# Performance work log

Measured on AMD Instinct MI355X. Metric: run time of the kernel, lower is better.

Reference implementation:

```python
import jax, jax.numpy as jnp
import numpy as np

LOOKUP_WINDOW = 101  # module init arg
EPS = 1e-12  # F.normalize eps


def setup_inputs() -> dict:
    key = jax.random.key(0)
    k1, k2, k3 = jax.random.split(key, 3)
    B, T, F_IN, D = 4, 2048, 2048, 128
    x = jax.random.normal(k1, (B, T, F_IN), dtype=jnp.float32)
    # nn.Linear(in_filters, output_dim); stored here as [in, out] so y = x @ W + b
    W = jax.random.normal(k2, (F_IN, D), dtype=jnp.float32) / np.sqrt(F_IN).astype(np.float32)
    b = jax.random.normal(k3, (D,), dtype=jnp.float32) * 0.01
    return {"x": x, "W": W, "b": b}


def reference(x, W, b):
    hw = LOOKUP_WINDOW // 2
    # projection + L2 normalize over feature dim (F.normalize p=2, dim=-1)
    p = x @ W + b  # [B,T,D]
    p = p / jnp.maximum(jnp.linalg.norm(p, axis=-1, keepdims=True), EPS)
    B, T, D = p.shape
    # zero-pad along time so out-of-range neighbors contribute 0 similarity
    pp = jnp.pad(p, ((0, 0), (hw, hw), (0, 0)))  # [B, T+2*hw, D]
    # window gather: idx[t, w] = t + w indexes padded time axis (neighbor t + w - hw)
    idx = jnp.arange(T)[:, None] + jnp.arange(LOOKUP_WINDOW)[None, :]  # [T, W]
    windows = pp[:, idx, :]  # [B, T, W, D]
    # banded similarity: sim[b,t,w] = <p[b,t], neighbor at offset w-hw>
    sim = jnp.einsum('btd,btwd->btw', p, windows)
    return sim  # [B, T, LOOKUP_WINDOW]
```

## Files before the change

kernel.cpp:

```cpp
#include <hip/hip_runtime.h>
#include <hip/hip_bf16.h>

#define T_LEN 2048
#define D_DIM 128
#define K_DIM 2048
#define M_DIM 8192
#define LOOKUP 101
#define HWIN 50

typedef __attribute__((ext_vector_type(8))) short short8;
typedef __attribute__((ext_vector_type(4))) float f32x4;

static __device__ __forceinline__ unsigned int f2bf(float f) {
  unsigned int u = __float_as_uint(f);
  return (u + 0x7fffu + ((u >> 16) & 1u)) >> 16;
}
static __device__ __forceinline__ float bflo(unsigned int u) { return __uint_as_float(u << 16); }
static __device__ __forceinline__ float bfhi(unsigned int u) { return __uint_as_float(u & 0xffff0000u); }

static __device__ __forceinline__ short8 pack8(float4 lo, float4 hi) {
  uint4 u;
  u.x = f2bf(lo.x) | (f2bf(lo.y) << 16);
  u.y = f2bf(lo.z) | (f2bf(lo.w) << 16);
  u.z = f2bf(hi.x) | (f2bf(hi.y) << 16);
  u.w = f2bf(hi.z) | (f2bf(hi.w) << 16);
  return *(short8*)&u;
}

typedef __attribute__((address_space(3))) unsigned char lds_uchar;
typedef const __attribute__((address_space(1))) unsigned char g_uchar;
static __device__ __forceinline__ void gll16(const void* g, void* l) {
  __builtin_amdgcn_global_load_lds((g_uchar*)g, (lds_uchar*)l, 16, 0, 0);
}

__global__ __launch_bounds__(256) void k_pack(const float* __restrict__ W,
                                              unsigned short* __restrict__ Bp) {
  __shared__ float sw[32][132];
  const int ks = blockIdx.x;
  const int t = threadIdx.x;
  const float* src = W + (size_t)ks * 32 * D_DIM;
#pragma unroll
  for (int j = 0; j < 4; ++j) {
    int idx = t + j * 256;
    int row = idx >> 5, c4 = idx & 31;
    float4 v = *(const float4*)(src + row * D_DIM + c4 * 4);
    *(float4*)&sw[row][c4 * 4] = v;
  }
  __syncthreads();
#pragma unroll
  for (int e = 0; e < 2; ++e) {
    int f = t * 2 + e;
    int ct = f >> 6, l = f & 63;
    int kr = (l >> 4) * 8, col = ct * 16 + (l & 15);
    uint4 o;
    o.x = f2bf(sw[kr + 0][col]) | (f2bf(sw[kr + 1][col]) << 16);
    o.y = f2bf(sw[kr + 2][col]) | (f2bf(sw[kr + 3][col]) << 16);
    o.z = f2bf(sw[kr + 4][col]) | (f2bf(sw[kr + 5][col]) << 16);
    o.w = f2bf(sw[kr + 6][col]) | (f2bf(sw[kr + 7][col]) << 16);
    *(uint4*)(Bp + (((size_t)(ks * 8 + ct) << 6) + l) * 8) = o;
  }
}

__global__ __launch_bounds__(512, 4) void k_gemm(const float* __restrict__ X,
                                                 const unsigned short* __restrict__ Bp,
                                                 const float* __restrict__ bias,
                                                 unsigned short* __restrict__ Pn) {
  __shared__ __align__(16) unsigned char smem[65536];
  const int tid = threadIdx.x;
  const int lane = tid & 63;
  const int wv = tid >> 6;
  const int r0 = blockIdx.x * 16;
  const int l15 = lane & 15;
  const int kg = lane >> 4;

  unsigned char* Ab = smem + wv * 8192;
  const int srow = lane >> 5;
  const int scol = lane & 31;

  f32x4 acc[8];
#pragma unroll
  for (int i = 0; i < 8; ++i) acc[i] = (f32x4){0.f, 0.f, 0.f, 0.f};

  for (int c = 0; c < 2; ++c) {
#pragma unroll
    for (int i = 0; i < 8; ++i) {
      int r = 2 * i + srow;
      int gsrc = scol ^ (r & 7);
      const float* src = X + (size_t)(r0 + r) * K_DIM + wv * 256 + c * 128 + gsrc * 4;
      gll16(src, Ab + i * 1024);
    }
    asm volatile("s_waitcnt vmcnt(0)" ::: "memory");
    __builtin_amdgcn_sched_barrier(0);
#pragma unroll
    for (int s = 0; s < 4; ++s) {
      int g0 = s * 8 + kg * 2;
      float4 alo = *(const float4*)(Ab + l15 * 512 + (((g0 + 0) ^ (l15 & 7)) << 4));
      float4 ahi = *(const float4*)(Ab + l15 * 512 + (((g0 + 1) ^ (l15 & 7)) << 4));
      short8 af = pack8(alo, ahi);
      int ksg = wv * 8 + c * 4 + s;
#pragma unroll
      for (int ct = 0; ct < 8; ++ct) {
        short8 bf = *(const short8*)(Bp + (((size_t)(ksg * 8 + ct) << 6) + lane) * 8);
        acc[ct] = __builtin_amdgcn_mfma_f32_16x16x32_bf16(af, bf, acc[ct], 0, 0, 0);
      }
    }
  }

  float* Pw = (float*)Ab;
#pragma unroll
  for (int ct = 0; ct < 8; ++ct)
#pragma unroll
    for (int j = 0; j < 4; ++j)
      Pw[(kg * 4 + j) * 128 + ct * 16 + l15] = acc[ct][j];
  __syncthreads();

  const int row = tid >> 5;
  const int c4 = tid & 31;
  float4 tot = make_float4(0.f, 0.f, 0.f, 0.f);
#pragma unroll
  for (int q = 0; q < 8; ++q) {
    float4 v = *(const float4*)(smem + q * 8192 + row * 512 + c4 * 16);
    tot.x += v.x; tot.y += v.y; tot.z += v.z; tot.w += v.w;
  }
  float4 bv = *(const float4*)(bias + c4 * 4);
  tot.x += bv.x; tot.y += bv.y; tot.z += bv.z; tot.w += bv.w;
  float ss = tot.x * tot.x + tot.y * tot.y + tot.z * tot.z + tot.w * tot.w;
  ss += __shfl_xor(ss, 1);
  ss += __shfl_xor(ss, 2);
  ss += __shfl_xor(ss, 4);
  ss += __shfl_xor(ss, 8);
  ss += __shfl_xor(ss, 16);
  float sc = 1.0f / fmaxf(sqrtf(ss), 1e-12f);
  unsigned int p0 = f2bf(tot.x * sc) | (f2bf(tot.y * sc) << 16);
  unsigned int p1 = f2bf(tot.z * sc) | (f2bf(tot.w * sc) << 16);
  *(uint2*)(Pn + (size_t)(r0 + row) * D_DIM + c4 * 4) = make_uint2(p0, p1);
}

#define SROWS 144

__global__ __launch_bounds__(256) void k_sim(const unsigned short* __restrict__ Pn,
                                             float* __restrict__ out) {
  __shared__ unsigned short sm[SROWS * D_DIM];
  const int bb = blockIdx.x >> 6;
  const int tb = blockIdx.x & 63;
  const int t0 = tb * 32;
  const int tid = threadIdx.x;

  for (int idx = tid; idx < SROWS * 16; idx += 256) {
    int i = idx >> 4, seg = idx & 15;
    int t = t0 - HWIN + i;
    uint4 val = make_uint4(0u, 0u, 0u, 0u);
    if (t >= 0 && t < T_LEN)
      val = *(const uint4*)(Pn + ((size_t)bb * T_LEN + t) * D_DIM + seg * 8);
    *(uint4*)&sm[i * D_DIM + ((seg ^ (i & 7)) << 3)] = val;
  }
  __syncthreads();

  const int lane = tid & 63;
  const int wv = tid >> 6;
  const int l15 = lane & 15;
  const int kg = lane >> 4;
  const int rt = wv >> 1;
  const int itp = wv & 1;

  short8 af[4];
  const int ia = HWIN + rt * 16 + l15;
#pragma unroll
  for (int ks = 0; ks < 4; ++ks) {
    int g = ks * 4 + kg;
    af[ks] = *(const short8*)&sm[ia * D_DIM + ((g ^ (ia & 7)) << 3)];
  }

  for (int it = itp; it < 9; it += 2) {
    f32x4 acc = (f32x4){0.f, 0.f, 0.f, 0.f};
    const int ib = it * 16 + l15;
#pragma unroll
    for (int ks = 0; ks < 4; ++ks) {
      int g = ks * 4 + kg;
      short8 bf = *(const short8*)&sm[ib * D_DIM + ((g ^ (ib & 7)) << 3)];
      acc = __builtin_amdgcn_mfma_f32_16x16x32_bf16(af[ks], bf, acc, 0, 0, 0);
    }
#pragma unroll
    for (int j = 0; j < 4; ++j) {
      int r = rt * 16 + kg * 4 + j;
      int w = ib - r;
      if (w >= 0 && w <= 100)
        out[((size_t)bb * T_LEN + t0 + r) * LOOKUP + w] = acc[j];
    }
  }
}

extern "C" void kernel_launch(void* const* d_in, const int* in_sizes, int n_in,
                              void* d_out, int out_size, void* d_ws, size_t ws_size,
                              hipStream_t stream) {
  (void)in_sizes; (void)n_in; (void)out_size; (void)ws_size;
  const float* x = (const float*)d_in[0];
  const float* W = (const float*)d_in[1];
  const float* b = (const float*)d_in[2];
  float* out = (float*)d_out;
  unsigned short* Bp = (unsigned short*)d_ws;
  unsigned short* Pn = Bp + (size_t)D_DIM * K_DIM;

  k_pack<<<64, 256, 0, stream>>>(W, Bp);
  k_gemm<<<M_DIM / 16, 512, 0, stream>>>(x, Bp, b, Pn);
  k_sim<<<4 * (T_LEN / 32), 256, 0, stream>>>(Pn, out);
}
```

Baseline: 34.33 us.

## Software-pipeline GEMM K-loop with double-buffered LDS and prefetched B fragments

Restructures the projection GEMM inner loop into a four-stage software pipeline. A tiles are double-buffered in LDS at 64-column granularity, and B fragments are loaded into two alternating register sets ahead of use, with explicit vmcnt waits and sched barriers. The goal is to overlap global loads of X and packed W with MFMA work instead of waiting on all loads before computing. It raises register pressure, and correctness depends on the hand-counted vmcnt thresholds matching the number of outstanding loads.

```diff
diff --git a/kernel.cpp b/kernel.cpp
--- a/kernel.cpp
+++ b/kernel.cpp
@@ -15,8 +15,6 @@
   unsigned int u = __float_as_uint(f);
   return (u + 0x7fffu + ((u >> 16) & 1u)) >> 16;
 }
-static __device__ __forceinline__ float bflo(unsigned int u) { return __uint_as_float(u << 16); }
-static __device__ __forceinline__ float bfhi(unsigned int u) { return __uint_as_float(u & 0xffff0000u); }
 
 static __device__ __forceinline__ short8 pack8(float4 lo, float4 hi) {
   uint4 u;
@@ -32,6 +30,7 @@
 static __device__ __forceinline__ void gll16(const void* g, void* l) {
   __builtin_amdgcn_global_load_lds((g_uchar*)g, (lds_uchar*)l, 16, 0, 0);
 }
+#define SB() __builtin_amdgcn_sched_barrier(0)
 
 __global__ __launch_bounds__(256) void k_pack(const float* __restrict__ W,
                                               unsigned short* __restrict__ Bp) {
@@ -74,37 +73,82 @@
   const int kg = lane >> 4;
 
   unsigned char* Ab = smem + wv * 8192;
-  const int srow = lane >> 5;
-  const int scol = lane & 31;
 
   f32x4 acc[8];
 #pragma unroll
   for (int i = 0; i < 8; ++i) acc[i] = (f32x4){0.f, 0.f, 0.f, 0.f};
 
-  for (int c = 0; c < 2; ++c) {
-#pragma unroll
-    for (int i = 0; i < 8; ++i) {
-      int r = 2 * i + srow;
-      int gsrc = scol ^ (r & 7);
-      const float* src = X + (size_t)(r0 + r) * K_DIM + wv * 256 + c * 128 + gsrc * 4;
-      gll16(src, Ab + i * 1024);
+  short8 bA0, bA1, bA2, bA3, bA4, bA5, bA6, bA7;
+  short8 bB0, bB1, bB2, bB3, bB4, bB5, bB6, bB7;
+
+  auto stage = [&](int c) {
+#pragma unroll
+    for (int i = 0; i < 4; ++i) {
+      int r = i * 4 + (lane >> 4);
+      int gsrc = (lane & 15) ^ (r & 7);
+      const float* src = X + (size_t)(r0 + r) * K_DIM + wv * 256 + c * 64 + gsrc * 4;
+      gll16(src, Ab + (c & 1) * 4096 + i * 1024);
     }
-    asm volatile("s_waitcnt vmcnt(0)" ::: "memory");
-    __builtin_amdgcn_sched_barrier(0);
-#pragma unroll
-    for (int s = 0; s < 4; ++s) {
-      int g0 = s * 8 + kg * 2;
-      float4 alo = *(const float4*)(Ab + l15 * 512 + (((g0 + 0) ^ (l15 & 7)) << 4));
-      float4 ahi = *(const float4*)(Ab + l15 * 512 + (((g0 + 1) ^ (l15 & 7)) << 4));
-      short8 af = pack8(alo, ahi);
-      int ksg = wv * 8 + c * 4 + s;
-#pragma unroll
-      for (int ct = 0; ct < 8; ++ct) {
-        short8 bf = *(const short8*)(Bp + (((size_t)(ksg * 8 + ct) << 6) + lane) * 8);
-        acc[ct] = __builtin_amdgcn_mfma_f32_16x16x32_bf16(af, bf, acc[ct], 0, 0, 0);
-      }
-    }
-  }
+  };
+#define LOADB(P, step)                                                                  \
+  {                                                                                     \
+    int ksg = wv * 8 + (step);                                                          \
+    P##0 = *(const short8*)(Bp + ((size_t)(ksg * 8 + 0) * 64 + lane) * 8);              \
+    P##1 = *(const short8*)(Bp + ((size_t)(ksg * 8 + 1) * 64 + lane) * 8);              \
+    P##2 = *(const short8*)(Bp + ((size_t)(ksg * 8 + 2) * 64 + lane) * 8);              \
+    P##3 = *(const short8*)(Bp + ((size_t)(ksg * 8 + 3) * 64 + lane) * 8);              \
+    P##4 = *(const short8*)(Bp + ((size_t)(ksg * 8 + 4) * 64 + lane) * 8);              \
+    P##5 = *(const short8*)(Bp + ((size_t)(ksg * 8 + 5) * 64 + lane) * 8);              \
+    P##6 = *(const short8*)(Bp + ((size_t)(ksg * 8 + 6) * 64 + lane) * 8);              \
+    P##7 = *(const short8*)(Bp + ((size_t)(ksg * 8 + 7) * 64 + lane) * 8);              \
+  }
+#define DOSTEP(P, c, s)                                                                  \
+  {                                                                                      \
+    int g0 = (s)*8 + kg * 2;                                                             \
+    const unsigned char* ab = Ab + ((c)&1) * 4096 + l15 * 256;                           \
+    float4 alo = *(const float4*)(ab + (((g0 + 0) ^ (l15 & 7)) << 4));                   \
+    float4 ahi = *(const float4*)(ab + (((g0 + 1) ^ (l15 & 7)) << 4));                   \
+    short8 af = pack8(alo, ahi);                                                         \
+    acc[0] = __builtin_amdgcn_mfma_f32_16x16x32_bf16(af, P##0, acc[0], 0, 0, 0);         \
+    acc[1] = __builtin_amdgcn_mfma_f32_16x16x32_bf16(af, P##1, acc[1], 0, 0, 0);         \
+    acc[2] = __builtin_amdgcn_mfma_f32_16x16x32_bf16(af, P##2, acc[2], 0, 0, 0);         \
+    acc[3] = __builtin_amdgcn_mfma_f32_16x16x32_bf16(af, P##3, acc[3], 0, 0, 0);         \
+    acc[4] = __builtin_amdgcn_mfma_f32_16x16x32_bf16(af, P##4, acc[4], 0, 0, 0);         \
+    acc[5] = __builtin_amdgcn_mfma_f32_16x16x32_bf16(af, P##5, acc[5], 0, 0, 0);         \
+    acc[6] = __builtin_amdgcn_mfma_f32_16x16x32_bf16(af, P##6, acc[6], 0, 0, 0);         \
+    acc[7] = __builtin_amdgcn_mfma_f32_16x16x32_bf16(af, P##7, acc[7], 0, 0, 0);         \
+  }
+
+  stage(0);
+  SB();
+  LOADB(bA, 0);
+  SB();
+
+  for (int c = 0; c < 3; ++c) {
+    LOADB(bB, 2 * c + 1);
+    SB();
+    stage(c + 1);
+    SB();
+    asm volatile("s_waitcnt vmcnt(12)" ::: "memory");
+    SB();
+    DOSTEP(bA, c, 0);
+    SB();
+    LOADB(bA, 2 * c + 2);
+    SB();
+    asm volatile("s_waitcnt vmcnt(12)" ::: "memory");
+    SB();
+    DOSTEP(bB, c, 1);
+    SB();
+  }
+  LOADB(bB, 7);
+  SB();
+  asm volatile("s_waitcnt vmcnt(8)" ::: "memory");
+  SB();
+  DOSTEP(bA, 3, 0);
+  SB();
+  asm volatile("s_waitcnt vmcnt(0)" ::: "memory");
+  SB();
+  DOSTEP(bB, 3, 1);
 
   float* Pw = (float*)Ab;
 #pragma unroll
```

After: 33.65 us. 2.0% less time.

## Load X directly into registers with prefetch, swap MFMA operands, swizzle partial sums

Applied to the files above, without the earlier changes.

The GEMM kernel stops staging X tiles into LDS via global_load_lds and instead has each lane load its own fp32 fragment straight from global memory. It software-pipelines those loads one k-step ahead, together with the packed W fragments. MFMA operands are swapped so the accumulator comes out transposed, which allows vectorized float4 partial-sum stores into a XOR-swizzled LDS layout for the cross-wave reduction. This removes the LDS round trip and the vmcnt(0) barrier on the X path, at the cost of more registers for double-buffered fragments and possibly less coalesced global reads.

```diff
diff --git a/kernel.cpp b/kernel.cpp
--- a/kernel.cpp
+++ b/kernel.cpp
@@ -15,8 +15,6 @@
   unsigned int u = __float_as_uint(f);
   return (u + 0x7fffu + ((u >> 16) & 1u)) >> 16;
 }
-static __device__ __forceinline__ float bflo(unsigned int u) { return __uint_as_float(u << 16); }
-static __device__ __forceinline__ float bfhi(unsigned int u) { return __uint_as_float(u & 0xffff0000u); }
 
 static __device__ __forceinline__ short8 pack8(float4 lo, float4 hi) {
   uint4 u;
@@ -25,12 +23,6 @@
   u.z = f2bf(hi.x) | (f2bf(hi.y) << 16);
   u.w = f2bf(hi.z) | (f2bf(hi.w) << 16);
   return *(short8*)&u;
-}
-
-typedef __attribute__((address_space(3))) unsigned char lds_uchar;
-typedef const __attribute__((address_space(1))) unsigned char g_uchar;
-static __device__ __forceinline__ void gll16(const void* g, void* l) {
-  __builtin_amdgcn_global_load_lds((g_uchar*)g, (lds_uchar*)l, 16, 0, 0);
 }
 
 __global__ __launch_bounds__(256) void k_pack(const float* __restrict__ W,
@@ -65,7 +57,7 @@
                                                  const unsigned short* __restrict__ Bp,
                                                  const float* __restrict__ bias,
                                                  unsigned short* __restrict__ Pn) {
-  __shared__ __align__(16) unsigned char smem[65536];
+  __shared__ __align__(16) unsigned char Pw[8 * 8192];
   const int tid = threadIdx.x;
   const int lane = tid & 63;
   const int wv = tid >> 6;
@@ -73,53 +65,57 @@
   const int l15 = lane & 15;
   const int kg = lane >> 4;
 
-  unsigned char* Ab = smem + wv * 8192;
-  const int srow = lane >> 5;
-  const int scol = lane & 31;
+  const float* xb = X + (size_t)(r0 + l15) * K_DIM + wv * 256 + kg * 8;
 
   f32x4 acc[8];
 #pragma unroll
   for (int i = 0; i < 8; ++i) acc[i] = (f32x4){0.f, 0.f, 0.f, 0.f};
 
-  for (int c = 0; c < 2; ++c) {
-#pragma unroll
-    for (int i = 0; i < 8; ++i) {
-      int r = 2 * i + srow;
-      int gsrc = scol ^ (r & 7);
-      const float* src = X + (size_t)(r0 + r) * K_DIM + wv * 256 + c * 128 + gsrc * 4;
-      gll16(src, Ab + i * 1024);
-    }
-    asm volatile("s_waitcnt vmcnt(0)" ::: "memory");
-    __builtin_amdgcn_sched_barrier(0);
-#pragma unroll
-    for (int s = 0; s < 4; ++s) {
-      int g0 = s * 8 + kg * 2;
-      float4 alo = *(const float4*)(Ab + l15 * 512 + (((g0 + 0) ^ (l15 & 7)) << 4));
-      float4 ahi = *(const float4*)(Ab + l15 * 512 + (((g0 + 1) ^ (l15 & 7)) << 4));
-      short8 af = pack8(alo, ahi);
-      int ksg = wv * 8 + c * 4 + s;
-#pragma unroll
-      for (int ct = 0; ct < 8; ++ct) {
-        short8 bf = *(const short8*)(Bp + (((size_t)(ksg * 8 + ct) << 6) + lane) * 8);
-        acc[ct] = __builtin_amdgcn_mfma_f32_16x16x32_bf16(af, bf, acc[ct], 0, 0, 0);
-      }
-    }
-  }
-
-  float* Pw = (float*)Ab;
+  float4 xc[2];
+  short8 wc[8];
+  xc[0] = *(const float4*)(xb);
+  xc[1] = *(const float4*)(xb + 4);
 #pragma unroll
   for (int ct = 0; ct < 8; ++ct)
-#pragma unroll
-    for (int j = 0; j < 4; ++j)
-      Pw[(kg * 4 + j) * 128 + ct * 16 + l15] = acc[ct][j];
+    wc[ct] = *(const short8*)(Bp + (((size_t)(wv * 8) * 8 + ct) * 64 + lane) * 8);
+
+#pragma unroll
+  for (int s = 0; s < 8; ++s) {
+    float4 xn[2];
+    short8 wn[8];
+    if (s < 7) {
+      xn[0] = *(const float4*)(xb + (s + 1) * 32);
+      xn[1] = *(const float4*)(xb + (s + 1) * 32 + 4);
+#pragma unroll
+      for (int ct = 0; ct < 8; ++ct)
+        wn[ct] = *(const short8*)(Bp + (((size_t)(wv * 8 + s + 1) * 8 + ct) * 64 + lane) * 8);
+    }
+    short8 xf = pack8(xc[0], xc[1]);
+#pragma unroll
+    for (int ct = 0; ct < 8; ++ct)
+      acc[ct] = __builtin_amdgcn_mfma_f32_16x16x32_bf16(wc[ct], xf, acc[ct], 0, 0, 0);
+    if (s < 7) {
+      xc[0] = xn[0]; xc[1] = xn[1];
+#pragma unroll
+      for (int ct = 0; ct < 8; ++ct) wc[ct] = wn[ct];
+    }
+  }
+
+  unsigned char* pwb = Pw + wv * 8192;
+#pragma unroll
+  for (int ct = 0; ct < 8; ++ct) {
+    int byte = l15 * 512 + ((ct * 64 + kg * 16) ^ ((l15 & 7) << 4));
+    *(float4*)(pwb + byte) = make_float4(acc[ct][0], acc[ct][1], acc[ct][2], acc[ct][3]);
+  }
   __syncthreads();
 
   const int row = tid >> 5;
   const int c4 = tid & 31;
+  const int rbyte = row * 512 + ((c4 * 16) ^ ((row & 7) << 4));
   float4 tot = make_float4(0.f, 0.f, 0.f, 0.f);
 #pragma unroll
   for (int q = 0; q < 8; ++q) {
-    float4 v = *(const float4*)(smem + q * 8192 + row * 512 + c4 * 16);
+    float4 v = *(const float4*)(Pw + q * 8192 + rbyte);
     tot.x += v.x; tot.y += v.y; tot.z += v.z; tot.w += v.w;
   }
   float4 bv = *(const float4*)(bias + c4 * 4);
```

Result: no change. 34.50 us (+0.5%).

## Restructure projection GEMM as pipelined K-loop with LDS ring buffer

Applied to the files above, without the earlier changes.

The GEMM kernel previously split K across 8 waves per 16-row block and reduced partial sums through LDS, with B fragments read straight from global memory. It now handles 32 rows per block and walks K in 64-wide chunks, staging both X and packed W tiles into a 4-slot LDS ring with async global-to-LDS loads kept two chunks ahead. Each wave owns a 16-row by 32-column output tile, so no cross-wave partial-sum reduction is needed before the bias, normalize and bf16 store. The cost is a long serial K loop with a barrier per chunk, and half as many blocks at lower occupancy.

```diff
diff --git a/kernel.cpp b/kernel.cpp
--- a/kernel.cpp
+++ b/kernel.cpp
@@ -15,8 +15,6 @@
   unsigned int u = __float_as_uint(f);
   return (u + 0x7fffu + ((u >> 16) & 1u)) >> 16;
 }
-static __device__ __forceinline__ float bflo(unsigned int u) { return __uint_as_float(u << 16); }
-static __device__ __forceinline__ float bfhi(unsigned int u) { return __uint_as_float(u & 0xffff0000u); }
 
 static __device__ __forceinline__ short8 pack8(float4 lo, float4 hi) {
   uint4 u;
@@ -61,79 +59,107 @@
   }
 }
 
-__global__ __launch_bounds__(512, 4) void k_gemm(const float* __restrict__ X,
+#define CHK 64
+#define NCHK (K_DIM / CHK)
+#define SLOT 24576
+
+__global__ __launch_bounds__(512, 2) void k_gemm(const float* __restrict__ X,
                                                  const unsigned short* __restrict__ Bp,
                                                  const float* __restrict__ bias,
                                                  unsigned short* __restrict__ Pn) {
-  __shared__ __align__(16) unsigned char smem[65536];
+  __shared__ __align__(16) unsigned char ring[4 * SLOT + 16384];
   const int tid = threadIdx.x;
   const int lane = tid & 63;
   const int wv = tid >> 6;
-  const int r0 = blockIdx.x * 16;
+  const int r0 = blockIdx.x * 32;
   const int l15 = lane & 15;
   const int kg = lane >> 4;
-
-  unsigned char* Ab = smem + wv * 8192;
-  const int srow = lane >> 5;
-  const int scol = lane & 31;
-
-  f32x4 acc[8];
-#pragma unroll
-  for (int i = 0; i < 8; ++i) acc[i] = (f32x4){0.f, 0.f, 0.f, 0.f};
-
-  for (int c = 0; c < 2; ++c) {
-#pragma unroll
-    for (int i = 0; i < 8; ++i) {
-      int r = 2 * i + srow;
-      int gsrc = scol ^ (r & 7);
-      const float* src = X + (size_t)(r0 + r) * K_DIM + wv * 256 + c * 128 + gsrc * 4;
-      gll16(src, Ab + i * 1024);
-    }
-    asm volatile("s_waitcnt vmcnt(0)" ::: "memory");
-    __builtin_amdgcn_sched_barrier(0);
-#pragma unroll
-    for (int s = 0; s < 4; ++s) {
-      int g0 = s * 8 + kg * 2;
-      float4 alo = *(const float4*)(Ab + l15 * 512 + (((g0 + 0) ^ (l15 & 7)) << 4));
-      float4 ahi = *(const float4*)(Ab + l15 * 512 + (((g0 + 1) ^ (l15 & 7)) << 4));
+  const int rg = wv >> 2;
+  const int wc = wv & 3;
+
+  f32x4 acc[2];
+  acc[0] = (f32x4){0.f, 0.f, 0.f, 0.f};
+  acc[1] = (f32x4){0.f, 0.f, 0.f, 0.f};
+
+  auto stage = [&](int cc) {
+    unsigned char* base = ring + (cc & 3) * SLOT;
+#pragma unroll
+    for (int u = 0; u < 3; ++u) {
+      int i = wv * 3 + u;
+      if (i < 8) {
+        int row = i * 4 + (lane >> 4);
+        int gs = (lane & 15) ^ (row & 15);
+        gll16(X + (size_t)(r0 + row) * K_DIM + cc * CHK + gs * 4, base + i * 1024);
+      } else {
+        int j = i - 8;
+        int ksg = cc * 2 + (j >> 3);
+        gll16(Bp + (((size_t)(ksg * 8 + (j & 7))) * 64 + lane) * 8, base + 8192 + j * 1024);
+      }
+    }
+  };
+
+  stage(0);
+  stage(1);
+  for (int c = 0; c < NCHK; ++c) {
+    if (c + 2 < NCHK) {
+      stage(c + 2);
+      asm volatile("s_waitcnt vmcnt(6)" ::: "memory");
+    } else if (c + 1 < NCHK) {
+      asm volatile("s_waitcnt vmcnt(3)" ::: "memory");
+    } else {
+      asm volatile("s_waitcnt vmcnt(0)" ::: "memory");
+    }
+    __builtin_amdgcn_s_barrier();
+    const unsigned char* Ab = ring + (c & 3) * SLOT;
+    const unsigned char* Bb = Ab + 8192;
+#pragma unroll
+    for (int s = 0; s < 2; ++s) {
+      int row = rg * 16 + l15;
+      int g = kg * 2 + s * 8;
+      float4 alo = *(const float4*)(Ab + row * 256 + ((g ^ (row & 15)) << 4));
+      float4 ahi = *(const float4*)(Ab + row * 256 + (((g + 1) ^ (row & 15)) << 4));
       short8 af = pack8(alo, ahi);
-      int ksg = wv * 8 + c * 4 + s;
-#pragma unroll
-      for (int ct = 0; ct < 8; ++ct) {
-        short8 bf = *(const short8*)(Bp + (((size_t)(ksg * 8 + ct) << 6) + lane) * 8);
-        acc[ct] = __builtin_amdgcn_mfma_f32_16x16x32_bf16(af, bf, acc[ct], 0, 0, 0);
-      }
-    }
-  }
-
-  float* Pw = (float*)Ab;
-#pragma unroll
-  for (int ct = 0; ct < 8; ++ct)
-#pragma unroll
-    for (int j = 0; j < 4; ++j)
-      Pw[(kg * 4 + j) * 128 + ct * 16 + l15] = acc[ct][j];
+      short8 w0 = *(const short8*)(Bb + ((s * 8 + wc * 2 + 0) * 64 + lane) * 16);
+      short8 w1 = *(const short8*)(Bb + ((s * 8 + wc * 2 + 1) * 64 + lane) * 16);
+      acc[0] = __builtin_amdgcn_mfma_f32_16x16x32_bf16(w0, af, acc[0], 0, 0, 0);
+      acc[1] = __builtin_amdgcn_mfma_f32_16x16x32_bf16(w1, af, acc[1], 0, 0, 0);
+    }
+  }
+
+  unsigned char* Pq = ring + 4 * SLOT;
+  {
+    int row = rg * 16 + l15;
+#pragma unroll
+    for (int ctl = 0; ctl < 2; ++ctl) {
+      int gq = (wc * 2 + ctl) * 4 + kg;
+      int byte = row * 512 + ((gq * 16) ^ ((row & 7) << 4));
+      *(float4*)(Pq + byte) = make_float4(acc[ctl][0], acc[ctl][1], acc[ctl][2], acc[ctl][3]);
+    }
+  }
   __syncthreads();
 
-  const int row = tid >> 5;
-  const int c4 = tid & 31;
-  float4 tot = make_float4(0.f, 0.f, 0.f, 0.f);
-#pragma unroll
-  for (int q = 0; q < 8; ++q) {
-    float4 v = *(const float4*)(smem + q * 8192 + row * 512 + c4 * 16);
-    tot.x += v.x; tot.y += v.y; tot.z += v.z; tot.w += v.w;
-  }
-  float4 bv = *(const float4*)(bias + c4 * 4);
-  tot.x += bv.x; tot.y += bv.y; tot.z += bv.z; tot.w += bv.w;
-  float ss = tot.x * tot.x + tot.y * tot.y + tot.z * tot.z + tot.w * tot.w;
+  const int row = tid >> 4;
+  const int c8 = tid & 15;
+  float4 v0 = *(const float4*)(Pq + row * 512 + (((2 * c8) * 16) ^ ((row & 7) << 4)));
+  float4 v1 = *(const float4*)(Pq + row * 512 + (((2 * c8 + 1) * 16) ^ ((row & 7) << 4)));
+  float4 bv0 = *(const float4*)(bias + c8 * 8);
+  float4 bv1 = *(const float4*)(bias + c8 * 8 + 4);
+  float tot[8] = {v0.x + bv0.x, v0.y + bv0.y, v0.z + bv0.z, v0.w + bv0.w,
+                  v1.x + bv1.x, v1.y + bv1.y, v1.z + bv1.z, v1.w + bv1.w};
+  float ss = 0.f;
+#pragma unroll
+  for (int i = 0; i < 8; ++i) ss += tot[i] * tot[i];
   ss += __shfl_xor(ss, 1);
   ss += __shfl_xor(ss, 2);
   ss += __shfl_xor(ss, 4);
   ss += __shfl_xor(ss, 8);
-  ss += __shfl_xor(ss, 16);
   float sc = 1.0f / fmaxf(sqrtf(ss), 1e-12f);
-  unsigned int p0 = f2bf(tot.x * sc) | (f2bf(tot.y * sc) << 16);
-  unsigned int p1 = f2bf(tot.z * sc) | (f2bf(tot.w * sc) << 16);
-  *(uint2*)(Pn + (size_t)(r0 + row) * D_DIM + c4 * 4) = make_uint2(p0, p1);
+  uint4 o;
+  o.x = f2bf(tot[0] * sc) | (f2bf(tot[1] * sc) << 16);
+  o.y = f2bf(tot[2] * sc) | (f2bf(tot[3] * sc) << 16);
+  o.z = f2bf(tot[4] * sc) | (f2bf(tot[5] * sc) << 16);
+  o.w = f2bf(tot[6] * sc) | (f2bf(tot[7] * sc) << 16);
+  *(uint4*)(Pn + (size_t)(r0 + row) * D_DIM + c8 * 8) = o;
 }
 
 #define SROWS 144
@@ -202,6 +228,6 @@
   unsigned short* Pn = Bp + (size_t)D_DIM * K_DIM;
 
   k_pack<<<64, 256, 0, stream>>>(W, Bp);
-  k_gemm<<<M_DIM / 16, 512, 0, stream>>>(x, Bp, b, Pn);
+  k_gemm<<<M_DIM / 32, 512, 0, stream>>>(x, Bp, b, Pn);
   k_sim<<<4 * (T_LEN / 32), 256, 0, stream>>>(Pn, out);
 }
```

New measurement: 40.05 us. +16.7%, slower.
